# Kernel tuning notes

Hardware: AMD Instinct MI355X
Metric: run time of the kernel (lower is better)

## Reference

```python
import jax, jax.numpy as jnp
import numpy as np

N = 100000
E = 3200000
NODE_F = 128
EDGE_F = 16
OUT_C = 15


def setup_inputs() -> dict:
    key = jax.random.key(0)
    k1, k2, k3, k4, k5 = jax.random.split(key, 5)
    x = jax.random.normal(k1, (N, NODE_F), dtype=jnp.float32)
    edge_index = jax.random.randint(k2, (2, E), 0, N, dtype=jnp.int64)
    edge_attr = jax.random.normal(k3, (E, EDGE_F), dtype=jnp.float32)
    # xavier-uniform parameters
    def xavier(k, shape):
        lim = (6.0 / (shape[0] + shape[1])) ** 0.5
        return jax.random.uniform(k, shape, dtype=jnp.float32, minval=-lim, maxval=lim)
    weight_node = xavier(k4, (NODE_F, OUT_C))
    weight_edge = xavier(k5, (EDGE_F, OUT_C))
    # sparse adjacency in COO form (same connectivity as edge_index, value 1.0)
    adj_values = jnp.ones((E,), dtype=jnp.float32)
    return {"x": x, "edge_index": edge_index, "edge_attr": edge_attr,
            "weight_node": weight_node, "weight_edge": weight_edge,
            "adj_values": adj_values}


def reference(x, edge_index, edge_attr, weight_node, weight_edge, adj_values):
    rows, cols = edge_index[0], edge_index[1]
    # SpMM: (A @ x)[i] = sum_{nnz with row i} val * x[col]   -> [N, NODE_F]
    ax = jax.ops.segment_sum(adj_values[:, None] * x[cols], rows, num_segments=N)
    axw = ax @ weight_node          # [N, OUT_C]
    ew = edge_attr @ weight_edge    # [E, OUT_C]
    # dropout is identity in eval mode
    # complex bilinear score: all imaginary parts are zero, conj is identity,
    # so Re(sum(h * e * conj(t))) == sum(h * e * t)
    heads = axw[rows]               # [E, OUT_C]
    tails = axw[cols]               # [E, OUT_C]
    raw_scores = jnp.sum(heads * ew * tails, axis=-1)  # [E]
    scores = jax.nn.sigmoid(raw_scores)
    return (axw, ew, scores)
```

## Files before the change

### kernel.cpp

```cpp
#include <hip/hip_runtime.h>
#include <math.h>

#define N_NODES 100000
#define N_EDGES 3200000
#define NODE_F  128
#define EDGE_F  16
#define OUT_C   15

__global__ __launch_bounds__(256) void node_proj_kernel(
    const float* __restrict__ x, const float* __restrict__ wn,
    float* __restrict__ xw)
{
    __shared__ float wl[NODE_F * OUT_C];
    const int tid = threadIdx.x;
    for (int i = tid; i < NODE_F * OUT_C; i += 256) wl[i] = wn[i];
    __syncthreads();

    const int n = blockIdx.x * 256 + tid;
    if (n >= N_NODES) return;

    float acc[OUT_C];
#pragma unroll
    for (int c = 0; c < OUT_C; ++c) acc[c] = 0.f;

    const float4* xr = (const float4*)(x + (size_t)n * NODE_F);
#pragma unroll 4
    for (int k4 = 0; k4 < NODE_F / 4; ++k4) {
        float4 v = xr[k4];
        const float* vp = &v.x;
#pragma unroll
        for (int j = 0; j < 4; ++j) {
            const float xv = vp[j];
            const int k = k4 * 4 + j;
#pragma unroll
            for (int c = 0; c < OUT_C; ++c)
                acc[c] = fmaf(xv, wl[k * OUT_C + c], acc[c]);
        }
    }

    float* out = xw + (size_t)n * OUT_C;
#pragma unroll
    for (int c = 0; c < OUT_C; ++c) out[c] = acc[c];
}

__global__ __launch_bounds__(256) void edge_scatter_kernel(
    const int* __restrict__ rows, const int* __restrict__ cols,
    const float* __restrict__ adj, const float* __restrict__ xw,
    float* __restrict__ axw)
{
    const int gid = blockIdx.x * 256 + threadIdx.x;
    const int e = gid >> 4;
    const int c = gid & 15;
    if (c >= OUT_C) return;

    const int r  = __builtin_nontemporal_load(rows + e);
    const int cl = __builtin_nontemporal_load(cols + e);
    const float a = __builtin_nontemporal_load(adj + e);
    const float v = a * xw[(size_t)cl * OUT_C + c];
    atomicAdd(&axw[(size_t)r * OUT_C + c], v);
}

__global__ __launch_bounds__(256) void edge_fused_kernel(
    const int* __restrict__ rows, const int* __restrict__ cols,
    const float* __restrict__ ea, const float* __restrict__ we,
    const float* __restrict__ axw,
    float* __restrict__ ew_out, float* __restrict__ scores)
{
    __shared__ float ws[EDGE_F * OUT_C];
    if (threadIdx.x < EDGE_F * OUT_C) ws[threadIdx.x] = we[threadIdx.x];
    __syncthreads();

    const int e = blockIdx.x * 256 + threadIdx.x;
    if (e >= N_EDGES) return;

    const float4* ear = (const float4*)(ea + (size_t)e * EDGE_F);
    float av[EDGE_F];
#pragma unroll
    for (int j = 0; j < 4; ++j) {
        float4 v = ear[j];
        av[4 * j + 0] = v.x; av[4 * j + 1] = v.y;
        av[4 * j + 2] = v.z; av[4 * j + 3] = v.w;
    }

    float ew[OUT_C];
#pragma unroll
    for (int c = 0; c < OUT_C; ++c) ew[c] = 0.f;
#pragma unroll
    for (int k = 0; k < EDGE_F; ++k) {
        const float a = av[k];
#pragma unroll
        for (int c = 0; c < OUT_C; ++c)
            ew[c] = fmaf(a, ws[k * OUT_C + c], ew[c]);
    }

    float* ewp = ew_out + (size_t)e * OUT_C;
#pragma unroll
    for (int c = 0; c < OUT_C; ++c) ewp[c] = ew[c];

    const int r  = rows[e];
    const int cl = cols[e];
    const float* h = axw + (size_t)r  * OUT_C;
    const float* t = axw + (size_t)cl * OUT_C;
    float s = 0.f;
#pragma unroll
    for (int c = 0; c < OUT_C; ++c)
        s += ew[c] * h[c] * t[c];

    scores[e] = 1.f / (1.f + expf(-s));
}

extern "C" void kernel_launch(void* const* d_in, const int* in_sizes, int n_in,
                              void* d_out, int out_size, void* d_ws, size_t ws_size,
                              hipStream_t stream) {
    const float* x    = (const float*)d_in[0];
    const int*   eidx = (const int*)d_in[1];
    const float* ea   = (const float*)d_in[2];
    const float* wn   = (const float*)d_in[3];
    const float* we   = (const float*)d_in[4];
    const float* adj  = (const float*)d_in[5];

    const int* rows = eidx;
    const int* cols = eidx + N_EDGES;

    float* out    = (float*)d_out;
    float* axw    = out;
    float* ew_out = out + (size_t)N_NODES * OUT_C;
    float* scores = out + (size_t)N_NODES * OUT_C
                        + (size_t)N_EDGES * OUT_C;

    float* xw = (float*)d_ws;

    hipMemsetAsync(axw, 0, (size_t)N_NODES * OUT_C * sizeof(float), stream);

    node_proj_kernel<<<(N_NODES + 255) / 256, 256, 0, stream>>>(x, wn, xw);

    edge_scatter_kernel<<<(N_EDGES * 16) / 256, 256, 0, stream>>>(
        rows, cols, adj, xw, axw);

    edge_fused_kernel<<<(N_EDGES + 255) / 256, 256, 0, stream>>>(
        rows, cols, ea, we, axw, ew_out, scores);
}
```

Measured before the change: 803.2 us.

## Replace atomic edge scatter with CSR build and per-node gather; stage ew stores

Builds a CSR layout every call: row histogram, a three-kernel prefix scan, then a binning scatter of (col, val) pairs. A per-node gather kernel then sums neighbours without float atomics, and the old atomic scatter is kept as a fallback when workspace is too small. The edge kernel stages its ew output in shared memory so global writes are coalesced vector stores, and uses nontemporal loads and stores. The extra passes and 3.2M int atomics for binning may cost as much as the float atomics they replace.

```diff
diff --git a/kernel.cpp b/kernel.cpp
--- a/kernel.cpp
+++ b/kernel.cpp
@@ -7,6 +7,11 @@
 #define EDGE_F  16
 #define OUT_C   15
 
+#define SCAN_B    1024
+#define SCAN_NBLK ((N_NODES + SCAN_B - 1) / SCAN_B)
+
+typedef float f32x4 __attribute__((ext_vector_type(4)));
+
 __global__ __launch_bounds__(256) void node_proj_kernel(
     const float* __restrict__ x, const float* __restrict__ wn,
     float* __restrict__ xw)
@@ -23,14 +28,13 @@
 #pragma unroll
     for (int c = 0; c < OUT_C; ++c) acc[c] = 0.f;
 
-    const float4* xr = (const float4*)(x + (size_t)n * NODE_F);
+    const f32x4* xr = (const f32x4*)(x + (size_t)n * NODE_F);
 #pragma unroll 4
     for (int k4 = 0; k4 < NODE_F / 4; ++k4) {
-        float4 v = xr[k4];
-        const float* vp = &v.x;
+        f32x4 v = xr[k4];
 #pragma unroll
         for (int j = 0; j < 4; ++j) {
-            const float xv = vp[j];
+            const float xv = v[j];
             const int k = k4 * 4 + j;
 #pragma unroll
             for (int c = 0; c < OUT_C; ++c)
@@ -41,6 +45,90 @@
     float* out = xw + (size_t)n * OUT_C;
 #pragma unroll
     for (int c = 0; c < OUT_C; ++c) out[c] = acc[c];
+}
+
+__global__ __launch_bounds__(256) void hist_kernel(
+    const int* __restrict__ rows, int* __restrict__ cnt)
+{
+    const int e = blockIdx.x * 256 + threadIdx.x;
+    if (e < N_EDGES) atomicAdd(&cnt[rows[e]], 1);
+}
+
+__global__ __launch_bounds__(SCAN_B) void scan_a_kernel(
+    const int* __restrict__ cnt, int* __restrict__ partials)
+{
+    __shared__ int s[SCAN_B];
+    const int i = blockIdx.x * SCAN_B + threadIdx.x;
+    s[threadIdx.x] = (i < N_NODES) ? cnt[i] : 0;
+    __syncthreads();
+    for (int st = SCAN_B / 2; st > 0; st >>= 1) {
+        if (threadIdx.x < st) s[threadIdx.x] += s[threadIdx.x + st];
+        __syncthreads();
+    }
+    if (threadIdx.x == 0) partials[blockIdx.x] = s[0];
+}
+
+__global__ void scan_b_kernel(const int* __restrict__ partials,
+                              int* __restrict__ block_off, int* __restrict__ off)
+{
+    if (threadIdx.x == 0 && blockIdx.x == 0) {
+        int acc = 0;
+        for (int b = 0; b < SCAN_NBLK; ++b) { block_off[b] = acc; acc += partials[b]; }
+        off[N_NODES] = acc;
+    }
+}
+
+__global__ __launch_bounds__(SCAN_B) void scan_c_kernel(
+    const int* __restrict__ cnt, const int* __restrict__ block_off,
+    int* __restrict__ off, int* __restrict__ cur)
+{
+    __shared__ int s[SCAN_B];
+    const int i = blockIdx.x * SCAN_B + threadIdx.x;
+    const int v = (i < N_NODES) ? cnt[i] : 0;
+    s[threadIdx.x] = v;
+    __syncthreads();
+    for (int st = 1; st < SCAN_B; st <<= 1) {
+        int t = (threadIdx.x >= st) ? s[threadIdx.x - st] : 0;
+        __syncthreads();
+        s[threadIdx.x] += t;
+        __syncthreads();
+    }
+    if (i < N_NODES) {
+        const int ex = block_off[blockIdx.x] + s[threadIdx.x] - v;
+        off[i] = ex;
+        cur[i] = ex;
+    }
+}
+
+__global__ __launch_bounds__(256) void scatter_bins_kernel(
+    const int* __restrict__ rows, const int* __restrict__ cols,
+    const float* __restrict__ adj, int* __restrict__ cur,
+    int2* __restrict__ bins)
+{
+    const int e = blockIdx.x * 256 + threadIdx.x;
+    if (e >= N_EDGES) return;
+    const int r   = __builtin_nontemporal_load(rows + e);
+    const int c   = __builtin_nontemporal_load(cols + e);
+    const float a = __builtin_nontemporal_load(adj + e);
+    const int pos = atomicAdd(&cur[r], 1);
+    bins[pos] = make_int2(c, __float_as_int(a));
+}
+
+__global__ __launch_bounds__(256) void gather_axw_kernel(
+    const int* __restrict__ off, const int2* __restrict__ bins,
+    const float* __restrict__ xw, float* __restrict__ axw)
+{
+    const int gid = blockIdx.x * 256 + threadIdx.x;
+    const int n = gid >> 4;
+    const int c = gid & 15;
+    if (c >= OUT_C) return;
+    const int start = off[n], end = off[n + 1];
+    float acc = 0.f;
+    for (int i = start; i < end; ++i) {
+        const int2 b = bins[i];
+        acc += __int_as_float(b.y) * xw[(size_t)b.x * OUT_C + c];
+    }
+    axw[(size_t)n * OUT_C + c] = acc;
 }
 
 __global__ __launch_bounds__(256) void edge_scatter_kernel(
@@ -52,12 +140,9 @@
     const int e = gid >> 4;
     const int c = gid & 15;
     if (c >= OUT_C) return;
-
-    const int r  = __builtin_nontemporal_load(rows + e);
-    const int cl = __builtin_nontemporal_load(cols + e);
-    const float a = __builtin_nontemporal_load(adj + e);
-    const float v = a * xw[(size_t)cl * OUT_C + c];
-    atomicAdd(&axw[(size_t)r * OUT_C + c], v);
+    const int r  = rows[e];
+    const int cl = cols[e];
+    atomicAdd(&axw[(size_t)r * OUT_C + c], adj[e] * xw[(size_t)cl * OUT_C + c]);
 }
 
 __global__ __launch_bounds__(256) void edge_fused_kernel(
@@ -67,19 +152,19 @@
     float* __restrict__ ew_out, float* __restrict__ scores)
 {
     __shared__ float ws[EDGE_F * OUT_C];
+    __shared__ float sew[256 * OUT_C];
     if (threadIdx.x < EDGE_F * OUT_C) ws[threadIdx.x] = we[threadIdx.x];
     __syncthreads();
 
     const int e = blockIdx.x * 256 + threadIdx.x;
-    if (e >= N_EDGES) return;
-
-    const float4* ear = (const float4*)(ea + (size_t)e * EDGE_F);
+
+    const f32x4* ear = (const f32x4*)(ea + (size_t)e * EDGE_F);
     float av[EDGE_F];
 #pragma unroll
     for (int j = 0; j < 4; ++j) {
-        float4 v = ear[j];
-        av[4 * j + 0] = v.x; av[4 * j + 1] = v.y;
-        av[4 * j + 2] = v.z; av[4 * j + 3] = v.w;
+        f32x4 v = __builtin_nontemporal_load(ear + j);
+        av[4 * j + 0] = v[0]; av[4 * j + 1] = v[1];
+        av[4 * j + 2] = v[2]; av[4 * j + 3] = v[3];
     }
 
     float ew[OUT_C];
@@ -93,9 +178,9 @@
             ew[c] = fmaf(a, ws[k * OUT_C + c], ew[c]);
     }
 
-    float* ewp = ew_out + (size_t)e * OUT_C;
-#pragma unroll
-    for (int c = 0; c < OUT_C; ++c) ewp[c] = ew[c];
+#pragma unroll
+    for (int c = 0; c < OUT_C; ++c)
+        sew[threadIdx.x * OUT_C + c] = ew[c];
 
     const int r  = rows[e];
     const int cl = cols[e];
@@ -105,9 +190,17 @@
 #pragma unroll
     for (int c = 0; c < OUT_C; ++c)
         s += ew[c] * h[c] * t[c];
-
-    scores[e] = 1.f / (1.f + expf(-s));
-}
+    __builtin_nontemporal_store(1.f / (1.f + expf(-s)), scores + e);
+
+    __syncthreads();
+
+    f32x4* dst4 = (f32x4*)(ew_out + (size_t)blockIdx.x * 256 * OUT_C);
+    const f32x4* src4 = (const f32x4*)sew;
+    for (int j = threadIdx.x; j < 256 * OUT_C / 4; j += 256)
+        __builtin_nontemporal_store(src4[j], dst4 + j);
+}
+
+static inline size_t align256(size_t x) { return (x + 255) & ~(size_t)255; }
 
 extern "C" void kernel_launch(void* const* d_in, const int* in_sizes, int n_in,
                               void* d_out, int out_size, void* d_ws, size_t ws_size,
@@ -128,15 +221,34 @@
     float* scores = out + (size_t)N_NODES * OUT_C
                         + (size_t)N_EDGES * OUT_C;
 
-    float* xw = (float*)d_ws;
-
-    hipMemsetAsync(axw, 0, (size_t)N_NODES * OUT_C * sizeof(float), stream);
+    char* w = (char*)d_ws;
+    float* xw = (float*)w;        w += align256((size_t)N_NODES * OUT_C * 4);
+    int* cnt = (int*)w;           w += align256((size_t)N_NODES * 4);
+    int* off = (int*)w;           w += align256((size_t)(N_NODES + 1) * 4);
+    int* cur = (int*)w;           w += align256((size_t)N_NODES * 4);
+    int* partials = (int*)w;      w += align256((size_t)SCAN_NBLK * 4);
+    int* block_off = (int*)w;     w += align256((size_t)SCAN_NBLK * 4);
+    int2* bins = (int2*)w;        w += (size_t)N_EDGES * sizeof(int2);
+    const size_t ws_needed = (size_t)(w - (char*)d_ws);
 
     node_proj_kernel<<<(N_NODES + 255) / 256, 256, 0, stream>>>(x, wn, xw);
 
-    edge_scatter_kernel<<<(N_EDGES * 16) / 256, 256, 0, stream>>>(
-        rows, cols, adj, xw, axw);
-
-    edge_fused_kernel<<<(N_EDGES + 255) / 256, 256, 0, stream>>>(
+    if (ws_size >= ws_needed) {
+        (void)hipMemsetAsync(cnt, 0, (size_t)N_NODES * 4, stream);
+        hist_kernel<<<(N_EDGES + 255) / 256, 256, 0, stream>>>(rows, cnt);
+        scan_a_kernel<<<SCAN_NBLK, SCAN_B, 0, stream>>>(cnt, partials);
+        scan_b_kernel<<<1, 64, 0, stream>>>(partials, block_off, off);
+        scan_c_kernel<<<SCAN_NBLK, SCAN_B, 0, stream>>>(cnt, block_off, off, cur);
+        scatter_bins_kernel<<<(N_EDGES + 255) / 256, 256, 0, stream>>>(
+            rows, cols, adj, cur, bins);
+        gather_axw_kernel<<<(N_NODES * 16) / 256, 256, 0, stream>>>(
+            off, bins, xw, axw);
+    } else {
+        (void)hipMemsetAsync(axw, 0, (size_t)N_NODES * OUT_C * 4, stream);
+        edge_scatter_kernel<<<(N_EDGES * 16) / 256, 256, 0, stream>>>(
+            rows, cols, adj, xw, axw);
+    }
+
+    edge_fused_kernel<<<N_EDGES / 256, 256, 0, stream>>>(
         rows, cols, ea, we, axw, ew_out, scores);
 }
```

After: 990.2 us. 23.3% more time.
